# Optimization experiments

Measured on AMD Instinct MI355X. Metric: run time of the kernel, lower is better.

## Reference

```python
import jax, jax.numpy as jnp
import numpy as np

H = 32        # query heads
KV = 8        # key/value heads
D = 128       # head_dim
GROUPS = H // KV
THETA = 10000.0


def _rope_cos_sin(position_ids):
    # position_ids: [B, S] int
    inv_freq = 1.0 / (THETA ** (jnp.arange(0, D, 2, dtype=jnp.float32) / D))  # [D/2]
    freqs = position_ids.astype(jnp.float32)[:, :, None] * inv_freq[None, None, :]  # [B,S,D/2]
    emb = jnp.concatenate([freqs, freqs], axis=-1)  # [B,S,D]
    return jnp.cos(emb), jnp.sin(emb)


def _rotate_half(x):
    x1, x2 = jnp.split(x, 2, axis=-1)
    return jnp.concatenate([-x2, x1], axis=-1)


def _apply_rope(x, cos, sin):
    # x: [B,h,S,D]; cos/sin: [B,S,D] -> broadcast over heads
    return x * cos[:, None, :, :] + _rotate_half(x) * sin[:, None, :, :]


def setup_inputs() -> dict:
    key = jax.random.key(0)
    ks = jax.random.split(key, 8)
    B, S, Dm = 2, 2048, 4096
    scale = lambda d: 1.0 / np.sqrt(d)
    hidden_states = jax.random.normal(ks[0], (B, S, Dm), dtype=jnp.float32)
    position_ids = jnp.broadcast_to(jnp.arange(S, dtype=jnp.int32)[None, :], (B, S))
    Wq = jax.random.normal(ks[1], (Dm, H * D), dtype=jnp.float32) * scale(Dm)
    Wk = jax.random.normal(ks[2], (Dm, KV * D), dtype=jnp.float32) * scale(Dm)
    Wv = jax.random.normal(ks[3], (Dm, KV * D), dtype=jnp.float32) * scale(Dm)
    Wo = jax.random.normal(ks[4], (H * D, Dm), dtype=jnp.float32) * scale(H * D)
    # per-head shift-encoder correction weights (small init so it's a correction)
    Ws_q = jax.random.normal(ks[5], (H, D, D), dtype=jnp.float32) * (0.02 * scale(D))
    Ws_k = jax.random.normal(ks[6], (H, D, D), dtype=jnp.float32) * (0.02 * scale(D))
    return {"hidden_states": hidden_states, "position_ids": position_ids,
            "Wq": Wq, "Wk": Wk, "Wv": Wv, "Wo": Wo, "Ws_q": Ws_q, "Ws_k": Ws_k}


def reference(hidden_states, position_ids, Wq, Wk, Wv, Wo, Ws_q, Ws_k):
    B, S, Dm = hidden_states.shape
    # projections -> [B, heads, S, D]
    q = (hidden_states @ Wq).reshape(B, S, H, D).transpose(0, 2, 1, 3)
    k = (hidden_states @ Wk).reshape(B, S, KV, D).transpose(0, 2, 1, 3)
    v = (hidden_states @ Wv).reshape(B, S, KV, D).transpose(0, 2, 1, 3)
    # RoPE
    cos, sin = _rope_cos_sin(position_ids)
    q = _apply_rope(q, cos, sin)
    k = _apply_rope(k, cos, sin)
    # GQA repeat_kv: [B,KV,S,D] -> [B,H,S,D]
    k = jnp.repeat(k, GROUPS, axis=1)
    v = jnp.repeat(v, GROUPS, axis=1)
    # causal SDPA
    scores = jnp.einsum('bhqd,bhkd->bhqk', q, k) / jnp.sqrt(jnp.float32(D))
    causal = jnp.tril(jnp.ones((S, S), dtype=bool))
    scores = jnp.where(causal[None, None, :, :], scores, jnp.float32(-1e30))
    probs = jax.nn.softmax(scores, axis=-1)
    attn = jnp.einsum('bhqk,bhkd->bhqd', probs, v)  # [B,H,S,D]
    attn = attn.transpose(0, 2, 1, 3)               # [B,S,H,D]
    # shift_encoder.do_shift: per-head linear correction from rotated Q and K
    delta = jnp.einsum('bhsd,hde->bshe', q, Ws_q) + jnp.einsum('bhsd,hde->bshe', k, Ws_k)
    attn = attn + delta
    # output projection
    out = attn.reshape(B, S, H * D) @ Wo
    return out
```

## Files before the change

kernel.cpp:

```cpp
#include <hip/hip_runtime.h>
#include <cstdint>

#define DEV __device__ __forceinline__

typedef __attribute__((ext_vector_type(4))) float  f32x4;
typedef __attribute__((ext_vector_type(8))) short  s16x8;
typedef __attribute__((ext_vector_type(4))) unsigned short u16x4;
typedef __attribute__((ext_vector_type(8))) unsigned short u16x8;

constexpr int B_   = 2;
constexpr int S_   = 2048;
constexpr int DM   = 4096;
constexpr int HQ   = 32;
constexpr int KVH  = 8;
constexpr int DH   = 128;
constexpr int NQKV = 6144;

DEV unsigned short f2bf(float f) {
  union { float f; unsigned u; } c; c.f = f;
  unsigned u = c.u + 0x7FFFu + ((c.u >> 16) & 1u);
  return (unsigned short)(u >> 16);
}
DEV float bf2f(unsigned short h) {
  union { unsigned u; float f; } c; c.u = (unsigned)h << 16; return c.f;
}
DEV void gload16(const void* g, const void* l) {
  __builtin_amdgcn_global_load_lds(
      (const __attribute__((address_space(1))) unsigned int*)(uintptr_t)g,
      (__attribute__((address_space(3))) unsigned int*)(unsigned)(uintptr_t)l,
      16, 0, 0);
}
DEV f32x4 mfma16x16(s16x8 a, s16x8 b, f32x4 c) {
  return __builtin_amdgcn_mfma_f32_16x16x32_bf16(a, b, c, 0, 0, 0);
}

__global__ __launch_bounds__(256) void k_tables(const int* __restrict__ pos,
                                                float* __restrict__ ct,
                                                float* __restrict__ st) {
  int i = blockIdx.x * 256 + threadIdx.x;
  if (i >= B_ * S_ * 64) return;
  int f = i & 63, bs = i >> 6;
  float p   = (float)pos[bs];
  float inv = __builtin_amdgcn_exp2f(-(float)f * 0.20762050593048355f);
  float a   = p * inv;
  ct[i] = cosf(a);
  st[i] = sinf(a);
}

__global__ __launch_bounds__(256) void k_cvt(const float* __restrict__ in,
                                             unsigned short* __restrict__ out,
                                             int n8) {
  int i = blockIdx.x * 256 + threadIdx.x;
  if (i >= n8) return;
  const f32x4* p = (const f32x4*)in + (size_t)2 * i;
  f32x4 a = p[0], b = p[1];
  u16x8 o;
  o[0] = f2bf(a[0]); o[1] = f2bf(a[1]); o[2] = f2bf(a[2]); o[3] = f2bf(a[3]);
  o[4] = f2bf(b[0]); o[5] = f2bf(b[1]); o[6] = f2bf(b[2]); o[7] = f2bf(b[3]);
  ((u16x8*)out)[i] = o;
}

__global__ __launch_bounds__(256) void k_tconv(const float* __restrict__ in,
                                               unsigned short* __restrict__ out,
                                               int R, int C,
                                               unsigned long long ibs,
                                               unsigned long long obs) {
  __shared__ float t[64][65];
  const int r0 = blockIdx.y * 64, c0 = blockIdx.x * 64;
  const float* ib = in + (size_t)blockIdx.z * ibs;
  unsigned short* ob = out + (size_t)blockIdx.z * obs;
  const int tid = threadIdx.x, tr = tid >> 4, c4 = (tid & 15) * 4;
#pragma unroll
  for (int it = 0; it < 4; ++it) {
    int rr = it * 16 + tr;
    f32x4 v = *(const f32x4*)&ib[(size_t)(r0 + rr) * C + (c0 + c4)];
    t[rr][c4 + 0] = v[0]; t[rr][c4 + 1] = v[1];
    t[rr][c4 + 2] = v[2]; t[rr][c4 + 3] = v[3];
  }
  __syncthreads();
#pragma unroll
  for (int it = 0; it < 4; ++it) {
    int cc = it * 16 + tr;
    u16x4 o;
    o[0] = f2bf(t[c4 + 0][cc]); o[1] = f2bf(t[c4 + 1][cc]);
    o[2] = f2bf(t[c4 + 2][cc]); o[3] = f2bf(t[c4 + 3][cc]);
    *(u16x4*)&ob[(size_t)(c0 + cc) * R + (r0 + c4)] = o;
  }
}

template <int BF16OUT, int SPLIT>
__global__ __launch_bounds__(512, 2) void k_gemm256(const unsigned short* __restrict__ A,
                                                    const unsigned short* __restrict__ BT,
                                                    void* __restrict__ Cv,
                                                    unsigned short* __restrict__ Pv,
                                                    int M, int N, int K, int NBX) {
  extern __shared__ __align__(16) char L[];
  const int tid = threadIdx.x;
  const int lane = tid & 63, w = tid >> 6;
  const int g = lane >> 4, ml = lane & 15;
  const int wr = w & 1, wc = w >> 1;

  int by, bx, koff, klen, cls = 0, ksl = 0;
  if (SPLIT) {
    const int sub = (int)blockIdx.x & 255;
    const int swz = (sub & 7) * 32 + (sub >> 3);
    cls = (int)blockIdx.x >> 8;
    if (cls == 0) { by = swz >> 4; bx = swz & 15; koff = 0; klen = K; }
    else {
      ksl = swz >> 7;
      int v = swz & 127;
      by = v >> 3; bx = 16 + (v & 7);
      koff = ksl * (K >> 1); klen = K >> 1;
    }
  } else {
    const int cpx = (int)gridDim.x >> 3;
    const int swz = ((int)blockIdx.x & 7) * cpx + ((int)blockIdx.x >> 3);
    by = swz / NBX; bx = swz - by * NBX; koff = 0; klen = K;
  }
  const int bm = by * 256, bn = bx * 256;

  const int srow_l = tid >> 3;
  const int scol_e = (((tid & 7) ^ ((tid >> 3) & 7)) << 3);
  const int nk = klen >> 6;

#define STAGE(kt, hf) do {                                                        \
    if ((kt) < nk) {                                                              \
      const unsigned short* sb; char* db;                                         \
      if ((hf) < 2) { sb = A  + (size_t)(bm + (hf) * 128) * K;                    \
                      db = L + ((kt) & 1) * 32768 + (hf) * 16384; }               \
      else          { sb = BT + (size_t)(bn + ((hf) - 2) * 128) * K;              \
                      db = L + 65536 + ((kt) & 1) * 32768 + ((hf) - 2) * 16384; } \
      sb += (size_t)koff + (size_t)(kt) * 64 + scol_e;                            \
      _Pragma("unroll")                                                           \
      for (int r_ = 0; r_ < 2; ++r_)                                              \
        gload16(sb + (size_t)(r_ * 64 + srow_l) * K, db + r_ * 8192 + w * 1024);  \
    } } while (0)

  f32x4 Z = {0.f, 0.f, 0.f, 0.f};
  f32x4 acc[8][4];
#pragma unroll
  for (int i = 0; i < 8; ++i)
#pragma unroll
    for (int j = 0; j < 4; ++j) acc[i][j] = Z;
  s16x8 bfr[4][2], afr[2][2];

#define FRAG(base, row, ks)                                                       \
  ((const s16x8*)((base) + ((((row) >> 7) * 16384 + ((row) & 127) * 128 +         \
                             ((ks) * 32 + 8 * g) * 2) ^ (((row) & 7) << 4))))

#define PHASE(q, kbuf, SKT, SHF, VM) do {                                         \
    if ((q) == 0) {                                                               \
      _Pragma("unroll")                                                           \
      for (int nf = 0; nf < 4; ++nf)                                              \
        _Pragma("unroll")                                                         \
        for (int ks = 0; ks < 2; ++ks)                                            \
          bfr[nf][ks] = *FRAG(L + 65536 + (kbuf) * 32768,                         \
                              wc * 64 + nf * 16 + ml, ks);                        \
    }                                                                             \
    _Pragma("unroll")                                                             \
    for (int mm = 0; mm < 2; ++mm)                                                \
      _Pragma("unroll")                                                           \
      for (int ks = 0; ks < 2; ++ks)                                              \
        afr[mm][ks] = *FRAG(L + (kbuf) * 32768,                                   \
                            32 * (2 * (q) + mm) + 16 * wr + ml, ks);              \
    STAGE(SKT, SHF);                                                              \
    if ((VM) == 1) { asm volatile("s_waitcnt vmcnt(6)" ::: "memory"); }           \
    else if ((VM) == 2) {                                                         \
      if (last) { asm volatile("s_waitcnt vmcnt(0)" ::: "memory"); }              \
      else      { asm volatile("s_waitcnt vmcnt(6)" ::: "memory"); }              \
    } else if ((VM) == 3) {                                                       \
      if (!last) { asm volatile("s_waitcnt vmcnt(6)" ::: "memory"); }             \
    }                                                                             \
    __builtin_amdgcn_s_barrier();                                                 \
    asm volatile("s_waitcnt lgkmcnt(0)" ::: "memory");                            \
    __builtin_amdgcn_sched_barrier(0);                                            \
    __builtin_amdgcn_s_setprio(1);                                                \
    _Pragma("unroll")                                                             \
    for (int mm = 0; mm < 2; ++mm)                                                \
      _Pragma("unroll")                                                           \
      for (int nf = 0; nf < 4; ++nf)                                              \
        _Pragma("unroll")                                                         \
        for (int ks = 0; ks < 2; ++ks)                                            \
          acc[2 * (q) + mm][nf] =                                                 \
              mfma16x16(afr[mm][ks], bfr[nf][ks], acc[2 * (q) + mm][nf]);         \
    __builtin_amdgcn_s_setprio(0);                                                \
    __builtin_amdgcn_s_barrier();                                                 \
  } while (0)

  STAGE(0, 0); STAGE(0, 1); STAGE(0, 2); STAGE(0, 3);
  STAGE(1, 2); STAGE(1, 3); STAGE(1, 0);
  asm volatile("s_waitcnt vmcnt(6)" ::: "memory");
  __builtin_amdgcn_s_barrier();

  const int iters = nk >> 1;
  for (int i = 0; i < iters; ++i) {
    const int t = 2 * i;
    const bool last = (i == iters - 1);
    PHASE(0, 0, t + 1, 1, 0);
    PHASE(1, 0, t + 2, 2, 0);
    PHASE(2, 0, t + 2, 0, 0);
    PHASE(3, 0, t + 2, 3, 2);
    PHASE(0, 1, t + 2, 1, 0);
    PHASE(1, 1, t + 3, 2, 0);
    PHASE(2, 1, t + 3, 3, 0);
    PHASE(3, 1, t + 3, 0, 3);
  }
#undef PHASE
#undef FRAG
#undef STAGE

  const int row0 = bm + 16 * wr + 4 * g, col0 = bn + wc * 64 + ml;
  const bool toPart = (SPLIT && cls == 1 && ksl == 1);
#pragma unroll
  for (int m = 0; m < 8; ++m)
#pragma unroll
    for (int nf = 0; nf < 4; ++nf)
#pragma unroll
      for (int r = 0; r < 4; ++r) {
        int row = row0 + 32 * m + r;
        int col = col0 + nf * 16;
        if (BF16OUT) {
          if (toPart)
            Pv[(size_t)row * 2048 + (col - 4096)] = f2bf(acc[m][nf][r]);
          else
            ((unsigned short*)Cv)[(size_t)row * N + col] = f2bf(acc[m][nf][r]);
        } else {
          ((float*)Cv)[(size_t)row * N + col] = acc[m][nf][r];
        }
      }
}

__global__ __launch_bounds__(256) void k_rope(const unsigned short* __restrict__ qkv,
                                              const unsigned short* __restrict__ p1,
                                              const float* __restrict__ ct,
                                              const float* __restrict__ st,
                                              unsigned short* __restrict__ qr,
                                              unsigned short* __restrict__ kr) {
  const int bs = blockIdx.x;
  const int b = bs >> 11, s = bs & 2047;
  const int tid = threadIdx.x;
  const float* cr = ct + (size_t)bs * 64;
  const float* sr = st + (size_t)bs * 64;
  const unsigned short* row = qkv + (size_t)bs * NQKV;
  {
    int h = tid >> 3, d0 = (tid & 7) * 16;
    u16x8 xs  = *(const u16x8*)&row[h * 128 + d0];
    u16x8 xs2 = *(const u16x8*)&row[h * 128 + d0 + 8];
    u16x8 xp  = *(const u16x8*)&row[h * 128 + (d0 ^ 64)];
    u16x8 xp2 = *(const u16x8*)&row[h * 128 + (d0 ^ 64) + 8];
    float sg = (d0 < 64) ? -1.f : 1.f;
    int ci = d0 & 63;
    u16x8 o1, o2;
#pragma unroll
    for (int j = 0; j < 8; ++j)
      o1[j] = f2bf(bf2f(xs[j]) * cr[ci + j] + sg * bf2f(xp[j]) * sr[ci + j]);
#pragma unroll
    for (int j = 0; j < 8; ++j)
      o2[j] = f2bf(bf2f(xs2[j]) * cr[ci + 8 + j] + sg * bf2f(xp2[j]) * sr[ci + 8 + j]);
    unsigned short* dst = qr + ((size_t)(b * HQ + h) * S_ + s) * DH + d0;
    *(u16x8*)dst = o1;
    *(u16x8*)(dst + 8) = o2;
  }
  if (tid < 64) {
    int kv = tid >> 3, d0 = (tid & 7) * 16;
    const unsigned short* krow = row + HQ * DH + kv * 128;
    const unsigned short* prow = p1 + (size_t)bs * 2048 + kv * 128;
    u16x8 xs  = *(const u16x8*)&krow[d0];
    u16x8 xs2 = *(const u16x8*)&krow[d0 + 8];
    u16x8 xp  = *(const u16x8*)&krow[d0 ^ 64];
    u16x8 xp2 = *(const u16x8*)&krow[(d0 ^ 64) + 8];
    u16x8 ys  = *(const u16x8*)&prow[d0];
    u16x8 ys2 = *(const u16x8*)&prow[d0 + 8];
    u16x8 yp  = *(const u16x8*)&prow[d0 ^ 64];
    u16x8 yp2 = *(const u16x8*)&prow[(d0 ^ 64) + 8];
    float sg = (d0 < 64) ? -1.f : 1.f;
    int ci = d0 & 63;
    u16x8 o1, o2;
#pragma unroll
    for (int j = 0; j < 8; ++j)
      o1[j] = f2bf((bf2f(xs[j]) + bf2f(ys[j])) * cr[ci + j] +
                   sg * (bf2f(xp[j]) + bf2f(yp[j])) * sr[ci + j]);
#pragma unroll
    for (int j = 0; j < 8; ++j)
      o2[j] = f2bf((bf2f(xs2[j]) + bf2f(ys2[j])) * cr[ci + 8 + j] +
                   sg * (bf2f(xp2[j]) + bf2f(yp2[j])) * sr[ci + 8 + j]);
    unsigned short* dst = kr + ((size_t)(b * KVH + kv) * S_ + s) * DH + d0;
    *(u16x8*)dst = o1;
    *(u16x8*)(dst + 8) = o2;
  }
}

__global__ __launch_bounds__(256) void k_vtrans(const unsigned short* __restrict__ qkv,
                                                const unsigned short* __restrict__ p1,
                                                unsigned short* __restrict__ vt) {
  __shared__ unsigned short t[64][65];
  const int z = blockIdx.z, b = z >> 3, kv = z & 7;
  const int s0 = blockIdx.x * 64, d0 = blockIdx.y * 64;
  const int tid = threadIdx.x, tr = tid >> 4, c4 = (tid & 15) * 4;
  const unsigned short* src = qkv + (size_t)(b * S_) * NQKV + HQ * DH + KVH * DH + kv * 128;
  const unsigned short* psr = p1 + (size_t)(b * S_) * 2048 + 1024 + kv * 128;
#pragma unroll
  for (int it = 0; it < 4; ++it) {
    int s = it * 16 + tr;
    u16x4 v = *(const u16x4*)&src[(size_t)(s0 + s) * NQKV + d0 + c4];
    u16x4 q = *(const u16x4*)&psr[(size_t)(s0 + s) * 2048 + d0 + c4];
    t[s][c4 + 0] = f2bf(bf2f(v[0]) + bf2f(q[0]));
    t[s][c4 + 1] = f2bf(bf2f(v[1]) + bf2f(q[1]));
    t[s][c4 + 2] = f2bf(bf2f(v[2]) + bf2f(q[2]));
    t[s][c4 + 3] = f2bf(bf2f(v[3]) + bf2f(q[3]));
  }
  __syncthreads();
  unsigned short* dst = vt + (size_t)(b * KVH + kv) * DH * S_;
#pragma unroll
  for (int it = 0; it < 4; ++it) {
    int d = it * 16 + tr;
    u16x4 o;
    o[0] = t[c4 + 0][d]; o[1] = t[c4 + 1][d];
    o[2] = t[c4 + 2][d]; o[3] = t[c4 + 3][d];
    *(u16x4*)&dst[(size_t)(d0 + d) * S_ + s0 + c4] = o;
  }
}

__global__ __launch_bounds__(256) void k_attn(const unsigned short* __restrict__ qr,
                                              const unsigned short* __restrict__ kr,
                                              const unsigned short* __restrict__ vt,
                                              const unsigned short* __restrict__ wsq,
                                              const unsigned short* __restrict__ wsk,
                                              unsigned short* __restrict__ att) {
  const int h = blockIdx.y, b = blockIdx.z, kvh = h >> 2;
  const int tid = threadIdx.x, lane = tid & 63, w = tid >> 6;
  const int g = lane >> 4, ml = lane & 15;

  __shared__ unsigned short kvbuf[16384];
  __shared__ unsigned short pbuf[4][32 * 68];
  unsigned short* kl = kvbuf;
  unsigned short* vl = kvbuf + 8192;

  const unsigned short* Kg = kr + (size_t)(b * KVH + kvh) * S_ * DH;
  const unsigned short* Vg = vt + (size_t)(b * KVH + kvh) * DH * S_;
  const float CS = 0.12751745f;
  f32x4 Z = {0.f, 0.f, 0.f, 0.f};

  for (int half = 0; half < 2; ++half) {
    const int qbx = half ? (15 - (int)blockIdx.x) : (int)blockIdx.x;
    const int qb0 = qbx * 128;
    const unsigned short* Qg = qr + ((size_t)(b * HQ + h) * S_ + qb0) * DH;

    __syncthreads();
#pragma unroll
    for (int it = 0; it < 8; ++it) {
      int c = w + 4 * it;
      int off = c * 1024 + lane * 16;
      int row = off >> 8;
      int sch = ((off >> 4) & 15) ^ (row & 7);
      gload16(Qg + (size_t)row * DH + sch * 8, (const char*)kvbuf + c * 1024);
    }
    __syncthreads();
    s16x8 qfr[2][4];
#pragma unroll
    for (int qf = 0; qf < 2; ++qf)
#pragma unroll
      for (int ds = 0; ds < 4; ++ds) {
        int row = 32 * w + 16 * qf + ml;
        int sch = (4 * ds + g) ^ (row & 7);
        qfr[qf][ds] = *(const s16x8*)((const char*)kvbuf + row * 256 + sch * 16);
      }

    float mstate[2] = {-3e30f, -3e30f};
    float lstate[2] = {0.f, 0.f};
    f32x4 oacc[2][8];
#pragma unroll
    for (int i = 0; i < 2; ++i)
#pragma unroll
      for (int j = 0; j < 8; ++j) oacc[i][j] = Z;

    const int ntiles = (qb0 >> 6) + 2;

    for (int t = 0; t < ntiles; ++t) {
      const int kv0 = t * 64;
      __syncthreads();
#pragma unroll
      for (int it = 0; it < 4; ++it) {
        int c = w + 4 * it;
        int off = c * 1024 + lane * 16;
        int row = off >> 8;
        int sch = ((off >> 4) & 15) ^ (row & 7);
        gload16(Kg + (size_t)(kv0 + row) * DH + sch * 8, (const char*)kl + c * 1024);
      }
#pragma unroll
      for (int it = 0; it < 4; ++it) {
        int c = w + 4 * it;
        int off = c * 1024 + lane * 16;
        int row = off >> 7;
        int sch = ((off >> 4) & 7) ^ (row & 7);
        gload16(Vg + (size_t)row * S_ + kv0 + sch * 8, (const char*)vl + c * 1024);
      }
      __syncthreads();

      f32x4 sacc[4][2];
#pragma unroll
      for (int i = 0; i < 4; ++i) { sacc[i][0] = Z; sacc[i][1] = Z; }
#pragma unroll
      for (int ds = 0; ds < 4; ++ds) {
        s16x8 af[4];
#pragma unroll
        for (int kf = 0; kf < 4; ++kf) {
          int row = 16 * kf + ml;
          int sch = (4 * ds + g) ^ (row & 7);
          af[kf] = *(const s16x8*)((const char*)kl + row * 256 + sch * 16);
        }
#pragma unroll
        for (int kf = 0; kf < 4; ++kf)
#pragma unroll
          for (int qf = 0; qf < 2; ++qf)
            sacc[kf][qf] = mfma16x16(af[kf], qfr[qf][ds], sacc[kf][qf]);
      }

      const int qg = qb0 + 32 * w + ml;
      const bool fullTile = (kv0 + 63 <= qb0 + 32 * w);
      float alpha[2];
#pragma unroll
      for (int qf = 0; qf < 2; ++qf) {
        int qq = qg + 16 * qf;
        float mx = -3e30f;
        if (fullTile) {
#pragma unroll
          for (int kf = 0; kf < 4; ++kf)
#pragma unroll
            for (int r = 0; r < 4; ++r) {
              float sv = sacc[kf][qf][r] * CS;
              sacc[kf][qf][r] = sv;
              mx = fmaxf(mx, sv);
            }
        } else {
#pragma unroll
          for (int kf = 0; kf < 4; ++kf)
#pragma unroll
            for (int r = 0; r < 4; ++r) {
              float sv = sacc[kf][qf][r] * CS;
              int kk = kv0 + 16 * kf + 4 * g + r;
              sv = (kk <= qq) ? sv : -3e30f;
              sacc[kf][qf][r] = sv;
              mx = fmaxf(mx, sv);
            }
        }
        mx = fmaxf(mx, __shfl_xor(mx, 16));
        mx = fmaxf(mx, __shfl_xor(mx, 32));
        float mn = fmaxf(mstate[qf], mx);
        alpha[qf] = __builtin_amdgcn_exp2f(mstate[qf] - mn);
        mstate[qf] = mn;
        float ls = 0.f;
#pragma unroll
        for (int kf = 0; kf < 4; ++kf) {
          u16x4 pk;
#pragma unroll
          for (int r = 0; r < 4; ++r) {
            float p = __builtin_amdgcn_exp2f(sacc[kf][qf][r] - mn);
            ls += p;
            pk[r] = f2bf(p);
          }
          *(u16x4*)&pbuf[w][(16 * qf + ml) * 68 + 16 * kf + 4 * g] = pk;
        }
        ls += __shfl_xor(ls, 16);
        ls += __shfl_xor(ls, 32);
        lstate[qf] = lstate[qf] * alpha[qf] + ls;
      }
#pragma unroll
      for (int mf = 0; mf < 2; ++mf)
#pragma unroll
        for (int r = 0; r < 4; ++r) {
          float a = __shfl(alpha[mf], (lane & 48) | (4 * g + r));
#pragma unroll
          for (int nf = 0; nf < 8; ++nf) oacc[mf][nf][r] *= a;
        }
#pragma unroll
      for (int ks = 0; ks < 2; ++ks) {
        s16x8 pa[2];
#pragma unroll
        for (int mf = 0; mf < 2; ++mf) {
          const unsigned short* pr = &pbuf[w][(16 * mf + ml) * 68 + 32 * ks + 8 * g];
          u16x4 lo = *(const u16x4*)pr;
          u16x4 hi = *(const u16x4*)(pr + 4);
          pa[mf] = (s16x8)__builtin_shufflevector(lo, hi, 0, 1, 2, 3, 4, 5, 6, 7);
        }
#pragma unroll
        for (int nf = 0; nf < 8; ++nf) {
          int row = 16 * nf + ml;
          int sch = (4 * ks + g) ^ (row & 7);
          s16x8 bv = *(const s16x8*)((const char*)vl + row * 128 + sch * 16);
#pragma unroll
          for (int mf = 0; mf < 2; ++mf)
            oacc[mf][nf] = mfma16x16(pa[mf], bv, oacc[mf][nf]);
        }
      }
    }

#pragma unroll
    for (int mf = 0; mf < 2; ++mf)
#pragma unroll
      for (int r = 0; r < 4; ++r) {
        float li = __shfl(lstate[mf], (lane & 48) | (4 * g + r));
        float inv = 1.0f / li;
#pragma unroll
        for (int nf = 0; nf < 8; ++nf) oacc[mf][nf][r] *= inv;
      }

    s16x8 kfr[2][4];
    __syncthreads();
#pragma unroll
    for (int it = 0; it < 8; ++it) {
      int c = w + 4 * it;
      int off = c * 1024 + lane * 16;
      int row = off >> 8;
      int sch = ((off >> 4) & 15) ^ (row & 7);
      gload16(Kg + (size_t)(qb0 + row) * DH + sch * 8, (const char*)kvbuf + c * 1024);
    }
    __syncthreads();
#pragma unroll
    for (int qf = 0; qf < 2; ++qf)
#pragma unroll
      for (int ds = 0; ds < 4; ++ds) {
        int row = 32 * w + 16 * qf + ml;
        int sch = (4 * ds + g) ^ (row & 7);
        kfr[qf][ds] = *(const s16x8*)((const char*)kvbuf + row * 256 + sch * 16);
      }

#pragma unroll
    for (int pass = 0; pass < 2; ++pass) {
      const unsigned short* Wg = (pass == 0 ? wsq : wsk) + (size_t)h * DH * DH;
      __syncthreads();
#pragma unroll
      for (int it = 0; it < 8; ++it) {
        int c = w + 4 * it;
        int off = c * 1024 + lane * 16;
        int row = off >> 8;
        int sch = ((off >> 4) & 15) ^ (row & 7);
        gload16(Wg + (size_t)row * DH + sch * 8, (const char*)kvbuf + c * 1024);
      }
      __syncthreads();
#pragma unroll
      for (int nf = 0; nf < 8; ++nf) {
        s16x8 wf[4];
#pragma unroll
        for (int ds = 0; ds < 4; ++ds) {
          int row = 16 * nf + ml;
          int sch = (4 * ds + g) ^ (row & 7);
          wf[ds] = *(const s16x8*)((const char*)kvbuf + row * 256 + sch * 16);
        }
#pragma unroll
        for (int qf = 0; qf < 2; ++qf)
#pragma unroll
          for (int ds = 0; ds < 4; ++ds)
            oacc[qf][nf] = mfma16x16(pass == 0 ? qfr[qf][ds] : kfr[qf][ds],
                                     wf[ds], oacc[qf][nf]);
      }
    }

#pragma unroll
    for (int mf = 0; mf < 2; ++mf)
#pragma unroll
      for (int r = 0; r < 4; ++r) {
        int rowg = b * S_ + qb0 + 32 * w + 16 * mf + 4 * g + r;
        size_t base = (size_t)rowg * (HQ * DH) + h * DH;
#pragma unroll
        for (int nf = 0; nf < 8; ++nf)
          att[base + 16 * nf + ml] = f2bf(oacc[mf][nf][r]);
      }
  }
}

extern "C" void kernel_launch(void* const* d_in, const int* in_sizes, int n_in,
                              void* d_out, int out_size, void* d_ws, size_t ws_size,
                              hipStream_t stream) {
  const float* hidden = (const float*)d_in[0];
  const int*   pos    = (const int*)d_in[1];
  const float* Wq     = (const float*)d_in[2];
  const float* Wk     = (const float*)d_in[3];
  const float* Wv     = (const float*)d_in[4];
  const float* Wo     = (const float*)d_in[5];
  const float* Wsq    = (const float*)d_in[6];
  const float* Wsk    = (const float*)d_in[7];

  char* ws = (char*)d_ws;
  unsigned short* XB    = (unsigned short*)(ws + 0);
  unsigned short* WQKVT = (unsigned short*)(ws + 33554432);
  unsigned short* WOT   = (unsigned short*)(ws + 83886080);
  unsigned short* P1    = WOT;
  unsigned short* WSQT  = (unsigned short*)(ws + 117440512);
  unsigned short* WSKT  = (unsigned short*)(ws + 118489088);
  float*          CT    = (float*)(ws + 119537664);
  float*          ST    = (float*)(ws + 120586240);
  unsigned short* QKV   = (unsigned short*)(ws + 121634816);
  unsigned short* QR    = (unsigned short*)(ws + 171966464);
  unsigned short* KR    = (unsigned short*)(ws + 205520896);
  unsigned short* VT    = (unsigned short*)(ws + 213909504);
  unsigned short* ATT   = (unsigned short*)(ws + 222298112);

  k_tables<<<1024, 256, 0, stream>>>(pos, CT, ST);
  k_cvt<<<8192, 256, 0, stream>>>(hidden, XB, 2097152);
  k_tconv<<<dim3(64, 64, 1), 256, 0, stream>>>(Wq, WQKVT, 4096, 4096, 0, 0);
  k_tconv<<<dim3(16, 64, 1), 256, 0, stream>>>(Wk, WQKVT + (size_t)4096 * 4096, 4096, 1024, 0, 0);
  k_tconv<<<dim3(16, 64, 1), 256, 0, stream>>>(Wv, WQKVT + (size_t)5120 * 4096, 4096, 1024, 0, 0);
  k_tconv<<<dim3(2, 2, 32), 256, 0, stream>>>(Wsq, WSQT, 128, 128, 16384, 16384);
  k_tconv<<<dim3(2, 2, 32), 256, 0, stream>>>(Wsk, WSKT, 128, 128, 16384, 16384);
  k_gemm256<1, 1><<<dim3(512), 512, 131072, stream>>>(XB, WQKVT, QKV, P1,
                                                      4096, 6144, 4096, 0);
  k_rope<<<4096, 256, 0, stream>>>(QKV, P1, CT, ST, QR, KR);
  k_vtrans<<<dim3(32, 2, 16), 256, 0, stream>>>(QKV, P1, VT);
  k_tconv<<<dim3(64, 64, 1), 256, 0, stream>>>(Wo, WOT, 4096, 4096, 0, 0);
  k_attn<<<dim3(8, 32, 2), 256, 0, stream>>>(QR, KR, VT, WSQT, WSKT, ATT);
  k_gemm256<0, 0><<<dim3(256), 512, 131072, stream>>>(ATT, WOT, d_out, nullptr,
                                                      4096, 4096, 4096, 16);
}
```

Measured before the change: 586.8 us.

## Register-prefetch next K/V tile in attention loop and set occupancy bound

Replaces the direct global-to-LDS loads of each K/V tile with a software pipeline. The next tile is loaded into registers while the current tile is being computed, then written into swizzled LDS at the start of the following iteration. The goal is to hide global memory latency behind the MFMA work. It also adds a min-blocks-per-CU launch bound of 2, which caps register use. The extra prefetch registers and the tighter bound may cause spills or lower occupancy.

```diff
diff --git a/kernel.cpp b/kernel.cpp
--- a/kernel.cpp
+++ b/kernel.cpp
@@ -321,12 +321,12 @@
   }
 }
 
-__global__ __launch_bounds__(256) void k_attn(const unsigned short* __restrict__ qr,
-                                              const unsigned short* __restrict__ kr,
-                                              const unsigned short* __restrict__ vt,
-                                              const unsigned short* __restrict__ wsq,
-                                              const unsigned short* __restrict__ wsk,
-                                              unsigned short* __restrict__ att) {
+__global__ __launch_bounds__(256, 2) void k_attn(const unsigned short* __restrict__ qr,
+                                                 const unsigned short* __restrict__ kr,
+                                                 const unsigned short* __restrict__ vt,
+                                                 const unsigned short* __restrict__ wsq,
+                                                 const unsigned short* __restrict__ wsk,
+                                                 unsigned short* __restrict__ att) {
   const int h = blockIdx.y, b = blockIdx.z, kvh = h >> 2;
   const int tid = threadIdx.x, lane = tid & 63, w = tid >> 6;
   const int g = lane >> 4, ml = lane & 15;
@@ -340,6 +340,7 @@
   const unsigned short* Vg = vt + (size_t)(b * KVH + kvh) * DH * S_;
   const float CS = 0.12751745f;
   f32x4 Z = {0.f, 0.f, 0.f, 0.f};
+  u16x8 pfk[4], pfv[4];
 
   for (int half = 0; half < 2; ++half) {
     const int qbx = half ? (15 - (int)blockIdx.x) : (int)blockIdx.x;
@@ -355,6 +356,12 @@
       int sch = ((off >> 4) & 15) ^ (row & 7);
       gload16(Qg + (size_t)row * DH + sch * 8, (const char*)kvbuf + c * 1024);
     }
+#pragma unroll
+    for (int i = 0; i < 4; ++i) {
+      int off = i * 4096 + tid * 16;
+      pfk[i] = *(const u16x8*)((const char*)Kg + (size_t)(off >> 8) * 256 + (off & 255));
+      pfv[i] = *(const u16x8*)((const char*)Vg + (size_t)(off >> 7) * 4096 + (off & 127));
+    }
     __syncthreads();
     s16x8 qfr[2][4];
 #pragma unroll
@@ -365,6 +372,7 @@
         int sch = (4 * ds + g) ^ (row & 7);
         qfr[qf][ds] = *(const s16x8*)((const char*)kvbuf + row * 256 + sch * 16);
       }
+    __syncthreads();
 
     float mstate[2] = {-3e30f, -3e30f};
     float lstate[2] = {0.f, 0.f};
@@ -378,22 +386,22 @@
 
     for (int t = 0; t < ntiles; ++t) {
       const int kv0 = t * 64;
-      __syncthreads();
-#pragma unroll
-      for (int it = 0; it < 4; ++it) {
-        int c = w + 4 * it;
-        int off = c * 1024 + lane * 16;
-        int row = off >> 8;
-        int sch = ((off >> 4) & 15) ^ (row & 7);
-        gload16(Kg + (size_t)(kv0 + row) * DH + sch * 8, (const char*)kl + c * 1024);
-      }
-#pragma unroll
-      for (int it = 0; it < 4; ++it) {
-        int c = w + 4 * it;
-        int off = c * 1024 + lane * 16;
-        int row = off >> 7;
-        int sch = ((off >> 4) & 7) ^ (row & 7);
-        gload16(Vg + (size_t)row * S_ + kv0 + sch * 8, (const char*)vl + c * 1024);
+#pragma unroll
+      for (int i = 0; i < 4; ++i) {
+        int off = i * 4096 + tid * 16;
+        int rk = off >> 8, ck = off & 255;
+        *(u16x8*)((char*)kl + rk * 256 + (ck ^ ((rk & 7) << 4))) = pfk[i];
+        int rv = off >> 7, cv = off & 127;
+        *(u16x8*)((char*)vl + rv * 128 + (cv ^ ((rv & 7) << 4))) = pfv[i];
+      }
+      if (t + 1 < ntiles) {
+        const int kv1 = kv0 + 64;
+#pragma unroll
+        for (int i = 0; i < 4; ++i) {
+          int off = i * 4096 + tid * 16;
+          pfk[i] = *(const u16x8*)((const char*)Kg + (size_t)(kv1 + (off >> 8)) * 256 + (off & 255));
+          pfv[i] = *(const u16x8*)((const char*)Vg + (size_t)(off >> 7) * 4096 + kv1 * 2 + (off & 127));
+        }
       }
       __syncthreads();
 
@@ -493,6 +501,7 @@
             oacc[mf][nf] = mfma16x16(pa[mf], bv, oacc[mf][nf]);
         }
       }
+      __syncthreads();
     }
 
 #pragma unroll
@@ -506,7 +515,6 @@
       }
 
     s16x8 kfr[2][4];
-    __syncthreads();
 #pragma unroll
     for (int it = 0; it < 8; ++it) {
       int c = w + 4 * it;
```

After: 552.0 us. 5.9% less time.
